# Optimization experiments

Hardware: AMD Instinct MI355X
Metric: run time of the kernel (lower is better)

## Reference

```python
import jax, jax.numpy as jnp
import numpy as np

I = 2048  # input_size
O = 2048  # output_size
K = 16    # number of parallel linears

def setup_inputs() -> dict:
    key = jax.random.key(0)
    ks = jax.random.split(key, 8)
    s_in = 1.0 / np.sqrt(I)
    s_cat = 1.0 / np.sqrt(K * O)
    x = jax.random.normal(ks[0], (4, 2048, I), dtype=jnp.float32)
    W16 = jax.random.uniform(ks[1], (K, O, I), jnp.float32, -s_in, s_in)   # stacked weights of 16 Linears
    b16 = jax.random.uniform(ks[2], (K, O), jnp.float32, -s_in, s_in)
    Wf = jax.random.uniform(ks[3], (O, K * O), jnp.float32, -s_cat, s_cat)  # fusion Linear weight
    bf = jax.random.uniform(ks[4], (O,), jnp.float32, -s_cat, s_cat)
    gamma = jnp.ones((O,), jnp.float32)  # LayerNorm weight
    beta = jnp.zeros((O,), jnp.float32)  # LayerNorm bias
    return {"x": x, "W16": W16, "b16": b16, "Wf": Wf, "bf": bf, "gamma": gamma, "beta": beta}

def reference(x, W16, b16, Wf, bf, gamma, beta):
    B, S, _ = x.shape
    # 16 parallel Linears as one batched GEMM; k index order == torch.cat order
    y = jnp.einsum('bsi,koi->bsko', x, W16) + b16          # [B,S,16,O]
    combined = y.reshape(B, S, K * O)                       # concat along last dim
    fused = jnp.einsum('bsc,oc->bso', combined, Wf) + bf    # fusion linear [B,S,O]
    # LayerNorm (eps=1e-5, torch default)
    mu = jnp.mean(fused, axis=-1, keepdims=True)
    var = jnp.mean(jnp.square(fused - mu), axis=-1, keepdims=True)
    normed = (fused - mu) * jax.lax.rsqrt(var + 1e-5) * gamma + beta
    # exact (erf) GELU matching torch nn.GELU default; dropout(p=0.005) is identity at eval
    return jax.nn.gelu(normed, approximate=False)
```

## Files before the change

kernel.cpp:

```cpp
#include <hip/hip_runtime.h>
#include <hip/hip_bf16.h>
#include <math.h>


typedef __bf16 bf16_t;
typedef __bf16 bf16x8 __attribute__((ext_vector_type(8)));
typedef __bf16 bf16x4 __attribute__((ext_vector_type(4)));
typedef float  f32x4  __attribute__((ext_vector_type(4)));

#define KC 32768
#define OD 2048
#define ID 2048
#define BSROWS 8192

#define GLL16(g, l) __builtin_amdgcn_global_load_lds( \
    (const __attribute__((address_space(1))) void*)(g), \
    (__attribute__((address_space(3))) void*)(l), 16, 0, 0)

__device__ __forceinline__ float wave_sum(float v) {
#pragma unroll
  for (int o = 32; o > 0; o >>= 1) v += __shfl_down(v, o, 64);
  return v;
}

__global__ __launch_bounds__(512, 1) void gemm256(
    const bf16_t* __restrict__ A, const bf16_t* __restrict__ B,
    float* __restrict__ C, int M, int N, int lda, int ldb,
    int Ks, int nbn, int mn)
{
  __shared__ char lds[131072];
  const int tid  = threadIdx.x;
  const int lane = tid & 63;
  const int wave = tid >> 6;

  const int nwg = gridDim.x;
  const int per = nwg >> 3;
  const int swz = (blockIdx.x & 7) * per + (blockIdx.x >> 3);
  const int z   = swz / mn;
  const int rem = swz - z * mn;
  const int bm  = (rem / nbn) * 256;
  const int bn  = (rem % nbn) * 256;
  const int k0  = z * Ks;
  float* Cz = C + (size_t)z * ((size_t)M * (size_t)N);

  const int wr = wave >> 2, wc = wave & 3;
  const int wrbase = wr * 128, wcbase = wc * 64;
  const int frow   = lane & 15;
  const int slot16 = (lane >> 4) * 16;

  const int srow = tid >> 2;
  const int scol = (tid & 3) * 8;
  const bf16_t* gA = A + (size_t)(bm + srow) * lda + k0 + scol;
  const bf16_t* gB = B + (size_t)(bn + srow) * ldb + k0 + scol;
  const int ldst = wave * 1024;

  f32x4 acc[8][4] = {};
  const int NC = Ks >> 5;

#define STAGE(c) do {                                             \
    char* Ab_ = lds + (((c) & 3) << 15);                          \
    char* Bb_ = Ab_ + 16384;                                      \
    const bf16_t* a_ = gA + (c) * 32;                             \
    const bf16_t* b_ = gB + (c) * 32;                             \
    GLL16(a_,                     Ab_ + ldst);                    \
    GLL16(a_ + (size_t)128 * lda, Ab_ + 8192 + ldst);             \
    GLL16(b_,                     Bb_ + ldst);                    \
    GLL16(b_ + (size_t)128 * ldb, Bb_ + 8192 + ldst);             \
  } while (0)

  STAGE(0); STAGE(1); STAGE(2);

  const int aoff = (wrbase + frow) * 64 + slot16;
  const int boff = (wcbase + frow) * 64 + slot16;

#pragma unroll 1
  for (int c = 0; c < NC; ++c) {
    if (c < NC - 2)       asm volatile("s_waitcnt vmcnt(8)" ::: "memory");
    else if (c == NC - 2) asm volatile("s_waitcnt vmcnt(4)" ::: "memory");
    else                  asm volatile("s_waitcnt vmcnt(0)" ::: "memory");
    __builtin_amdgcn_s_barrier();

    const char* ap = lds + ((c & 3) << 15) + aoff;
    const char* bp = lds + ((c & 3) << 15) + 16384 + boff;
    bf16x8 af[8], bg[4];
#pragma unroll
    for (int n = 0; n < 4; ++n)
      bg[n] = *reinterpret_cast<const bf16x8*>(bp + n * 1024);
#pragma unroll
    for (int m = 0; m < 8; ++m)
      af[m] = *reinterpret_cast<const bf16x8*>(ap + m * 1024);

    if (c + 3 < NC) STAGE(c + 3);

    __builtin_amdgcn_s_setprio(1);
#pragma unroll
    for (int m = 0; m < 8; ++m)
#pragma unroll
      for (int n = 0; n < 4; ++n)
        acc[m][n] = __builtin_amdgcn_mfma_f32_16x16x32_bf16(af[m], bg[n], acc[m][n], 0, 0, 0);
    __builtin_amdgcn_s_setprio(0);
  }
#undef STAGE

  const int cr = (lane >> 4) * 4, cc = lane & 15;
#pragma unroll
  for (int m = 0; m < 8; ++m)
#pragma unroll
    for (int n = 0; n < 4; ++n) {
      size_t base = (size_t)(bm + wrbase + m * 16 + cr) * N + (bn + wcbase + n * 16 + cc);
#pragma unroll
      for (int j = 0; j < 4; ++j)
        Cz[base + (size_t)j * N] = acc[m][n][j];
    }
}

__global__ void conv_wf_beq(const float* __restrict__ Wf, const float* __restrict__ b16,
                            bf16_t* __restrict__ Wf16, float* __restrict__ beq)
{
  const int o  = blockIdx.y;
  const int cb = blockIdx.x * 2048;
  const int t  = threadIdx.x;
  const size_t gbase = (size_t)o * KC + cb + t * 8;
  const float4 v0 = *(const float4*)(Wf + gbase);
  const float4 v1 = *(const float4*)(Wf + gbase + 4);
  const float4 b0 = *(const float4*)(b16 + cb + t * 8);
  const float4 b1 = *(const float4*)(b16 + cb + t * 8 + 4);
  bf16x8 r;
  r[0] = (bf16_t)v0.x; r[1] = (bf16_t)v0.y; r[2] = (bf16_t)v0.z; r[3] = (bf16_t)v0.w;
  r[4] = (bf16_t)v1.x; r[5] = (bf16_t)v1.y; r[6] = (bf16_t)v1.z; r[7] = (bf16_t)v1.w;
  *reinterpret_cast<bf16x8*>(Wf16 + gbase) = r;
  float s = v0.x * b0.x + v0.y * b0.y + v0.z * b0.z + v0.w * b0.w
          + v1.x * b1.x + v1.y * b1.y + v1.z * b1.z + v1.w * b1.w;
  s = wave_sum(s);
  __shared__ float red[4];
  if ((t & 63) == 0) red[t >> 6] = s;
  __syncthreads();
  if (t == 0) atomicAdd(beq + o, red[0] + red[1] + red[2] + red[3]);
}

__global__ void transpose_w16(const float* __restrict__ W, bf16_t* __restrict__ T)
{
  __shared__ bf16_t tile[64][65];
  const int cb = blockIdx.x * 64;
  const int ib = blockIdx.y * 64;
  const int tx = threadIdx.x & 63;
  const int ty = threadIdx.x >> 6;
#pragma unroll
  for (int r = ty; r < 64; r += 4)
    tile[r][tx] = (bf16_t)W[(size_t)(cb + r) * ID + ib + tx];
  __syncthreads();
#pragma unroll
  for (int r = ty; r < 64; r += 4)
    T[(size_t)(ib + r) * KC + cb + tx] = tile[tx][r];
}

__global__ void conv_x(const float* __restrict__ X, bf16_t* __restrict__ X16)
{
  const size_t i = ((size_t)blockIdx.x * 256 + threadIdx.x) * 8;
  const float4 v0 = *(const float4*)(X + i);
  const float4 v1 = *(const float4*)(X + i + 4);
  bf16x8 r;
  r[0] = (bf16_t)v0.x; r[1] = (bf16_t)v0.y; r[2] = (bf16_t)v0.z; r[3] = (bf16_t)v0.w;
  r[4] = (bf16_t)v1.x; r[5] = (bf16_t)v1.y; r[6] = (bf16_t)v1.z; r[7] = (bf16_t)v1.w;
  *reinterpret_cast<bf16x8*>(X16 + i) = r;
}

__global__ void reduce_weq(const float* __restrict__ slabs, bf16_t* __restrict__ Weq)
{
  const size_t MN = (size_t)OD * ID;
  const size_t i = ((size_t)blockIdx.x * 256 + threadIdx.x) * 4;
  float4 a = *(const float4*)(slabs + i);
  float4 b = *(const float4*)(slabs + MN + i);
  float4 c = *(const float4*)(slabs + 2 * MN + i);
  float4 d = *(const float4*)(slabs + 3 * MN + i);
  bf16x4 r;
  r[0] = (bf16_t)(a.x + b.x + c.x + d.x);
  r[1] = (bf16_t)(a.y + b.y + c.y + d.y);
  r[2] = (bf16_t)(a.z + b.z + c.z + d.z);
  r[3] = (bf16_t)(a.w + b.w + c.w + d.w);
  *reinterpret_cast<bf16x4*>(Weq + i) = r;
}

__global__ __launch_bounds__(256) void ln_gelu(
    const float* __restrict__ fused, const float* __restrict__ beq,
    const float* __restrict__ bfv, const float* __restrict__ gamma,
    const float* __restrict__ beta, float* __restrict__ out)
{
  const int row = blockIdx.x;
  const int t = threadIdx.x;
  const float* fr = fused + (size_t)row * OD;
  const int c0 = t * 8;
  float v[8];
  float s = 0.f, ss = 0.f;
#pragma unroll
  for (int j = 0; j < 2; ++j) {
    float4 x  = *(const float4*)(fr  + c0 + j * 4);
    float4 bq = *(const float4*)(beq + c0 + j * 4);
    float4 bb = *(const float4*)(bfv + c0 + j * 4);
    v[j * 4 + 0] = x.x + bq.x + bb.x;
    v[j * 4 + 1] = x.y + bq.y + bb.y;
    v[j * 4 + 2] = x.z + bq.z + bb.z;
    v[j * 4 + 3] = x.w + bq.w + bb.w;
#pragma unroll
    for (int e = 0; e < 4; ++e) { float w = v[j * 4 + e]; s += w; ss += w * w; }
  }
  s = wave_sum(s); ss = wave_sum(ss);
  __shared__ float rs[4], rss[4];
  if ((t & 63) == 0) { rs[t >> 6] = s; rss[t >> 6] = ss; }
  __syncthreads();
  const float S  = rs[0] + rs[1] + rs[2] + rs[3];
  const float SS = rss[0] + rss[1] + rss[2] + rss[3];
  const float mu   = S * (1.f / OD);
  const float var  = SS * (1.f / OD) - mu * mu;
  const float rstd = rsqrtf(var + 1e-5f);
#pragma unroll
  for (int j = 0; j < 2; ++j) {
    float4 g  = *(const float4*)(gamma + c0 + j * 4);
    float4 be = *(const float4*)(beta  + c0 + j * 4);
    float4 o;
    float xn;
    xn  = (v[j * 4 + 0] - mu) * rstd * g.x + be.x; o.x = 0.5f * xn * (1.f + erff(xn * 0.70710678118f));
    xn  = (v[j * 4 + 1] - mu) * rstd * g.y + be.y; o.y = 0.5f * xn * (1.f + erff(xn * 0.70710678118f));
    xn  = (v[j * 4 + 2] - mu) * rstd * g.z + be.z; o.z = 0.5f * xn * (1.f + erff(xn * 0.70710678118f));
    xn  = (v[j * 4 + 3] - mu) * rstd * g.w + be.w; o.w = 0.5f * xn * (1.f + erff(xn * 0.70710678118f));
    *(float4*)(out + (size_t)row * OD + c0 + j * 4) = o;
  }
}

extern "C" void kernel_launch(void* const* d_in, const int* in_sizes, int n_in,
                              void* d_out, int out_size, void* d_ws, size_t ws_size,
                              hipStream_t stream) {
  const float* x     = (const float*)d_in[0];
  const float* W16   = (const float*)d_in[1];
  const float* b16   = (const float*)d_in[2];
  const float* Wf    = (const float*)d_in[3];
  const float* bfv   = (const float*)d_in[4];
  const float* gamma = (const float*)d_in[5];
  const float* beta  = (const float*)d_in[6];
  float* out = (float*)d_out;

  char* ws = (char*)d_ws;
  bf16_t* W16T  = (bf16_t*)(ws);
  bf16_t* Wf16  = (bf16_t*)(ws + 134217728);
  bf16_t* X16   = (bf16_t*)(ws + 268435456);
  bf16_t* Weq   = (bf16_t*)(ws + 301989888);
  float*  beq   = (float*)(ws + 310378496);
  float*  slabs = (float*)(ws + 310386688);
  float*  fused = slabs;

  hipMemsetAsync(beq, 0, OD * sizeof(float), stream);

  conv_wf_beq<<<dim3(16, 2048), 256, 0, stream>>>(Wf, b16, Wf16, beq);
  transpose_w16<<<dim3(KC / 64, ID / 64), 256, 0, stream>>>(W16, W16T);
  conv_x<<<(BSROWS * ID) / (256 * 8), 256, 0, stream>>>(x, X16);

  gemm256<<<256, 512, 0, stream>>>(Wf16, W16T, slabs, OD, ID, KC, KC, KC / 4, 8, 64);
  reduce_weq<<<(OD * ID) / (256 * 4), 256, 0, stream>>>(slabs, Weq);

  gemm256<<<256, 512, 0, stream>>>(X16, Weq, fused, BSROWS, OD, ID, ID, ID, 8, 256);

  ln_gelu<<<BSROWS, 256, 0, stream>>>(fused, beq, bfv, gamma, beta, out);
}
```

Baseline: 623.7 us.

## Double-buffer LDS fragment reads in registers and deepen the global prefetch to four stages

The GEMM main loop now reads the next k-chunk's A/B fragments from LDS into a second register set while the MFMAs run on the current set. The global-to-LDS prefetch distance grows from three to four chunks, using all four LDS buffers, and the wait counts are adjusted to match. The aim is to hide LDS read latency behind MFMA work and keep more global loads in flight. In exchange it uses more VGPRs for the extra fragment set, and the loop assumes an even chunk count.

```diff
diff --git a/kernel.cpp b/kernel.cpp
--- a/kernel.cpp
+++ b/kernel.cpp
@@ -55,51 +55,68 @@
   const int ldst = wave * 1024;
 
   f32x4 acc[8][4] = {};
+  bf16x8 afA[8], bgA[4], afB[8], bgB[4];
   const int NC = Ks >> 5;
+
+  const int aoff = (wrbase + frow) * 64 + slot16;
+  const int boff = (wcbase + frow) * 64 + slot16;
 
 #define STAGE(c) do {                                             \
     char* Ab_ = lds + (((c) & 3) << 15);                          \
     char* Bb_ = Ab_ + 16384;                                      \
-    const bf16_t* a_ = gA + (c) * 32;                             \
-    const bf16_t* b_ = gB + (c) * 32;                             \
+    const bf16_t* a_ = gA + (size_t)(c) * 32;                     \
+    const bf16_t* b_ = gB + (size_t)(c) * 32;                     \
     GLL16(a_,                     Ab_ + ldst);                    \
     GLL16(a_ + (size_t)128 * lda, Ab_ + 8192 + ldst);             \
     GLL16(b_,                     Bb_ + ldst);                    \
     GLL16(b_ + (size_t)128 * ldb, Bb_ + 8192 + ldst);             \
   } while (0)
 
-  STAGE(0); STAGE(1); STAGE(2);
-
-  const int aoff = (wrbase + frow) * 64 + slot16;
-  const int boff = (wcbase + frow) * 64 + slot16;
+#define READ(c, af, bg) do {                                      \
+    const char* ap_ = lds + (((c) & 3) << 15) + aoff;             \
+    const char* bp_ = lds + (((c) & 3) << 15) + 16384 + boff;     \
+    _Pragma("unroll")                                             \
+    for (int n = 0; n < 4; ++n)                                   \
+      bg[n] = *reinterpret_cast<const bf16x8*>(bp_ + n * 1024);   \
+    _Pragma("unroll")                                             \
+    for (int m = 0; m < 8; ++m)                                   \
+      af[m] = *reinterpret_cast<const bf16x8*>(ap_ + m * 1024);   \
+  } while (0)
+
+#define MFMA32(af, bg) do {                                       \
+    __builtin_amdgcn_s_setprio(1);                                \
+    _Pragma("unroll")                                             \
+    for (int m = 0; m < 8; ++m)                                   \
+      _Pragma("unroll")                                           \
+      for (int n = 0; n < 4; ++n)                                 \
+        acc[m][n] = __builtin_amdgcn_mfma_f32_16x16x32_bf16(      \
+            af[m], bg[n], acc[m][n], 0, 0, 0);                    \
+    __builtin_amdgcn_s_setprio(0);                                \
+  } while (0)
+
+#define PHASE(c, afC, bgC, afN, bgN) do {                         \
+    if ((c) < NC - 3)       asm volatile("s_waitcnt vmcnt(8)" ::: "memory"); \
+    else if ((c) == NC - 3) asm volatile("s_waitcnt vmcnt(4)" ::: "memory"); \
+    else if ((c) == NC - 2) asm volatile("s_waitcnt vmcnt(0)" ::: "memory"); \
+    __builtin_amdgcn_s_barrier();                                 \
+    if ((c) + 4 < NC) STAGE((c) + 4);                             \
+    if ((c) + 1 < NC) READ((c) + 1, afN, bgN);                    \
+    MFMA32(afC, bgC);                                             \
+  } while (0)
+
+  STAGE(0); STAGE(1); STAGE(2); STAGE(3);
+  asm volatile("s_waitcnt vmcnt(12)" ::: "memory");
+  __builtin_amdgcn_s_barrier();
+  READ(0, afA, bgA);
 
 #pragma unroll 1
-  for (int c = 0; c < NC; ++c) {
-    if (c < NC - 2)       asm volatile("s_waitcnt vmcnt(8)" ::: "memory");
-    else if (c == NC - 2) asm volatile("s_waitcnt vmcnt(4)" ::: "memory");
-    else                  asm volatile("s_waitcnt vmcnt(0)" ::: "memory");
-    __builtin_amdgcn_s_barrier();
-
-    const char* ap = lds + ((c & 3) << 15) + aoff;
-    const char* bp = lds + ((c & 3) << 15) + 16384 + boff;
-    bf16x8 af[8], bg[4];
-#pragma unroll
-    for (int n = 0; n < 4; ++n)
-      bg[n] = *reinterpret_cast<const bf16x8*>(bp + n * 1024);
-#pragma unroll
-    for (int m = 0; m < 8; ++m)
-      af[m] = *reinterpret_cast<const bf16x8*>(ap + m * 1024);
-
-    if (c + 3 < NC) STAGE(c + 3);
-
-    __builtin_amdgcn_s_setprio(1);
-#pragma unroll
-    for (int m = 0; m < 8; ++m)
-#pragma unroll
-      for (int n = 0; n < 4; ++n)
-        acc[m][n] = __builtin_amdgcn_mfma_f32_16x16x32_bf16(af[m], bg[n], acc[m][n], 0, 0, 0);
-    __builtin_amdgcn_s_setprio(0);
+  for (int c = 0; c < NC; c += 2) {
+    PHASE(c,     afA, bgA, afB, bgB);
+    PHASE(c + 1, afB, bgB, afA, bgA);
   }
+#undef PHASE
+#undef MFMA32
+#undef READ
 #undef STAGE
 
   const int cr = (lane >> 4) * 4, cc = lane & 15;
```

New measurement: 600.3 us. 1.04x faster.

## Restructure GEMM main loop into 64-wide K tiles with phased LDS pipeline and swizzle

Applied to the files above, without the earlier changes.

The bf16 GEMM main loop moves from 32-wide K chunks with a 4-deep buffer to 64-wide K tiles, double-buffered in LDS. Each tile is processed in four phases that interleave global-to-LDS staging, register prefetch of the next A fragments and MFMAs, with an XOR-swizzled LDS layout meant to avoid bank conflicts. Separately, the weight transpose kernel now writes 16-byte vectorized rows instead of scalar bf16 stores. The aim is better overlap of memory and matrix work and fewer LDS conflicts, at the cost of more barriers per tile and more complex waitcnt logic that is easy to get wrong.

```diff
diff --git a/kernel.cpp b/kernel.cpp
--- a/kernel.cpp
+++ b/kernel.cpp
@@ -13,6 +13,11 @@
 #define ID 2048
 #define BSROWS 8192
 
+#define SEG_ALO 0
+#define SEG_AHI 16384
+#define SEG_BLO 32768
+#define SEG_BHI 49152
+
 #define GLL16(g, l) __builtin_amdgcn_global_load_lds( \
     (const __attribute__((address_space(1))) void*)(g), \
     (__attribute__((address_space(3))) void*)(l), 16, 0, 0)
@@ -35,73 +40,138 @@
 
   const int nwg = gridDim.x;
   const int per = nwg >> 3;
-  const int swz = (blockIdx.x & 7) * per + (blockIdx.x >> 3);
-  const int z   = swz / mn;
-  const int rem = swz - z * mn;
+  const int swzb = (blockIdx.x & 7) * per + (blockIdx.x >> 3);
+  const int z   = swzb / mn;
+  const int rem = swzb - z * mn;
   const int bm  = (rem / nbn) * 256;
   const int bn  = (rem % nbn) * 256;
   const int k0  = z * Ks;
   float* Cz = C + (size_t)z * ((size_t)M * (size_t)N);
 
   const int wr = wave >> 2, wc = wave & 3;
+  const int frow = lane & 15;
+
+  const int rdsl0 = ((((lane >> 4))    ^ (lane & 7)) * 16);
+  const int rdsl1 = ((((lane >> 4) + 4) ^ (lane & 7)) * 16);
+
+  const int srow8 = lane >> 3;
+  const int scole = ((lane & 7) ^ srow8) * 8;
+  const bf16_t* gAs = A + (size_t)(bm + srow8) * lda + k0 + scole;
+  const bf16_t* gBs = B + (size_t)(bn + srow8) * ldb + k0 + scole;
+
+  const int abase = wr * 16384 + frow * 128;
+  const int bbase = 32768 + (wc >> 1) * 16384 + ((wc & 1) * 64 + frow) * 128;
+
+  f32x4 acc[8][4] = {};
+  bf16x8 aA[2][2], aB[2][2], bA[4][2], bB[4][2];
+  const int NT = Ks >> 6;
+
+#define STAGEH(g, ld, segoff, tile, halfbase) do {                        \
+    const bf16_t* s_ = (g) + (size_t)((halfbase) + 16 * wave) * (ld)      \
+                           + (size_t)(tile) * 64;                         \
+    char* d_ = lds + (((tile) & 1) << 16) + (segoff) + wave * 2048;       \
+    GLL16(s_,                    d_);                                     \
+    GLL16(s_ + (size_t)8 * (ld), d_ + 1024);                              \
+  } while (0)
+
+#define READA(tile, q, ar) do {                                           \
+    const char* p_ = lds + (((tile) & 1) << 16) + abase + (q) * 4096;     \
+    _Pragma("unroll") for (int mh = 0; mh < 2; ++mh) {                    \
+      ar[mh][0] = *reinterpret_cast<const bf16x8*>(p_ + mh*2048 + rdsl0); \
+      ar[mh][1] = *reinterpret_cast<const bf16x8*>(p_ + mh*2048 + rdsl1); \
+    }                                                                     \
+  } while (0)
+
+#define READB(tile, bg) do {                                              \
+    const char* p_ = lds + (((tile) & 1) << 16) + bbase;                  \
+    _Pragma("unroll") for (int n = 0; n < 4; ++n) {                       \
+      bg[n][0] = *reinterpret_cast<const bf16x8*>(p_ + n*2048 + rdsl0);   \
+      bg[n][1] = *reinterpret_cast<const bf16x8*>(p_ + n*2048 + rdsl1);   \
+    }                                                                     \
+  } while (0)
+
+#define MFMAQ(p, ac, bc) do {                                             \
+    __builtin_amdgcn_s_setprio(1);                                        \
+    _Pragma("unroll") for (int mh = 0; mh < 2; ++mh)                      \
+      _Pragma("unroll") for (int n = 0; n < 4; ++n) {                     \
+        acc[2*(p)+mh][n] = __builtin_amdgcn_mfma_f32_16x16x32_bf16(       \
+            ac[mh][0], bc[n][0], acc[2*(p)+mh][n], 0, 0, 0);              \
+        acc[2*(p)+mh][n] = __builtin_amdgcn_mfma_f32_16x16x32_bf16(       \
+            ac[mh][1], bc[n][1], acc[2*(p)+mh][n], 0, 0, 0);              \
+      }                                                                   \
+    __builtin_amdgcn_s_setprio(0);                                        \
+  } while (0)
+
+#define ENDPH() do {                                                      \
+    asm volatile("s_waitcnt lgkmcnt(0)" ::: "memory");                    \
+    __builtin_amdgcn_sched_barrier(0);                                    \
+    __builtin_amdgcn_s_barrier();                                         \
+  } while (0)
+
+#define PH0(t, ac, an, bc) do {                                           \
+    if ((t) + 2 < NT) STAGEH(gBs, ldb, SEG_BLO, (t)+2, 0);                \
+    READA((t), 1, an);                                                    \
+    MFMAQ(0, ac, bc);                                                     \
+    ENDPH();                                                              \
+  } while (0)
+#define PH1(t, ac, an, bc) do {                                           \
+    if ((t) + 2 < NT) STAGEH(gBs, ldb, SEG_BHI, (t)+2, 128);              \
+    READA((t), 2, an);                                                    \
+    MFMAQ(1, ac, bc);                                                     \
+    ENDPH();                                                              \
+  } while (0)
+#define PH2(t, ac, an, bc) do {                                           \
+    READA((t), 3, an);                                                    \
+    MFMAQ(2, ac, bc);                                                     \
+    ENDPH();                                                              \
+  } while (0)
+#define PH3(t, ac, an, bc, bn) do {                                       \
+    if ((t) + 1 < NT) {                                                   \
+      if ((t) + 2 < NT) asm volatile("s_waitcnt vmcnt(4)" ::: "memory");  \
+      else              asm volatile("s_waitcnt vmcnt(0)" ::: "memory");  \
+      __builtin_amdgcn_s_barrier();   \
+    }                                                                     \
+    if ((t) + 2 < NT) { STAGEH(gAs, lda, SEG_ALO, (t)+2, 0);              \
+                        STAGEH(gAs, lda, SEG_AHI, (t)+2, 128); }          \
+    if ((t) + 1 < NT) { READA((t)+1, 0, an); READB((t)+1, bn); }          \
+    MFMAQ(3, ac, bc);                                                     \
+    ENDPH();                                                              \
+  } while (0)
+
+  STAGEH(gBs, ldb, SEG_BLO, 0, 0);   STAGEH(gBs, ldb, SEG_BHI, 0, 128);
+  STAGEH(gAs, lda, SEG_ALO, 0, 0);   STAGEH(gAs, lda, SEG_AHI, 0, 128);
+  STAGEH(gBs, ldb, SEG_BLO, 1, 0);   STAGEH(gBs, ldb, SEG_BHI, 1, 128);
+  STAGEH(gAs, lda, SEG_ALO, 1, 0);   STAGEH(gAs, lda, SEG_AHI, 1, 128);
+  asm volatile("s_waitcnt vmcnt(8)" ::: "memory");
+  __builtin_amdgcn_s_barrier();
+  READB(0, bA);
+  READA(0, 0, aA);
+  asm volatile("s_waitcnt lgkmcnt(0)" ::: "memory");
+  __builtin_amdgcn_sched_barrier(0);
+  __builtin_amdgcn_s_barrier();
+
+#pragma unroll 1
+  for (int t = 0; t < NT; t += 2) {
+    PH0(t,     aA, aB, bA);
+    PH1(t,     aB, aA, bA);
+    PH2(t,     aA, aB, bA);
+    PH3(t,     aB, aA, bA, bB);
+    PH0(t + 1, aA, aB, bB);
+    PH1(t + 1, aB, aA, bB);
+    PH2(t + 1, aA, aB, bB);
+    PH3(t + 1, aB, aA, bB, bA);
+  }
+#undef PH0
+#undef PH1
+#undef PH2
+#undef PH3
+#undef ENDPH
+#undef MFMAQ
+#undef READB
+#undef READA
+#undef STAGEH
+
   const int wrbase = wr * 128, wcbase = wc * 64;
-  const int frow   = lane & 15;
-  const int slot16 = (lane >> 4) * 16;
-
-  const int srow = tid >> 2;
-  const int scol = (tid & 3) * 8;
-  const bf16_t* gA = A + (size_t)(bm + srow) * lda + k0 + scol;
-  const bf16_t* gB = B + (size_t)(bn + srow) * ldb + k0 + scol;
-  const int ldst = wave * 1024;
-
-  f32x4 acc[8][4] = {};
-  const int NC = Ks >> 5;
-
-#define STAGE(c) do {                                             \
-    char* Ab_ = lds + (((c) & 3) << 15);                          \
-    char* Bb_ = Ab_ + 16384;                                      \
-    const bf16_t* a_ = gA + (c) * 32;                             \
-    const bf16_t* b_ = gB + (c) * 32;                             \
-    GLL16(a_,                     Ab_ + ldst);                    \
-    GLL16(a_ + (size_t)128 * lda, Ab_ + 8192 + ldst);             \
-    GLL16(b_,                     Bb_ + ldst);                    \
-    GLL16(b_ + (size_t)128 * ldb, Bb_ + 8192 + ldst);             \
-  } while (0)
-
-  STAGE(0); STAGE(1); STAGE(2);
-
-  const int aoff = (wrbase + frow) * 64 + slot16;
-  const int boff = (wcbase + frow) * 64 + slot16;
-
-#pragma unroll 1
-  for (int c = 0; c < NC; ++c) {
-    if (c < NC - 2)       asm volatile("s_waitcnt vmcnt(8)" ::: "memory");
-    else if (c == NC - 2) asm volatile("s_waitcnt vmcnt(4)" ::: "memory");
-    else                  asm volatile("s_waitcnt vmcnt(0)" ::: "memory");
-    __builtin_amdgcn_s_barrier();
-
-    const char* ap = lds + ((c & 3) << 15) + aoff;
-    const char* bp = lds + ((c & 3) << 15) + 16384 + boff;
-    bf16x8 af[8], bg[4];
-#pragma unroll
-    for (int n = 0; n < 4; ++n)
-      bg[n] = *reinterpret_cast<const bf16x8*>(bp + n * 1024);
-#pragma unroll
-    for (int m = 0; m < 8; ++m)
-      af[m] = *reinterpret_cast<const bf16x8*>(ap + m * 1024);
-
-    if (c + 3 < NC) STAGE(c + 3);
-
-    __builtin_amdgcn_s_setprio(1);
-#pragma unroll
-    for (int m = 0; m < 8; ++m)
-#pragma unroll
-      for (int n = 0; n < 4; ++n)
-        acc[m][n] = __builtin_amdgcn_mfma_f32_16x16x32_bf16(af[m], bg[n], acc[m][n], 0, 0, 0);
-    __builtin_amdgcn_s_setprio(0);
-  }
-#undef STAGE
-
   const int cr = (lane >> 4) * 4, cc = lane & 15;
 #pragma unroll
   for (int m = 0; m < 8; ++m)
@@ -149,9 +219,16 @@
   for (int r = ty; r < 64; r += 4)
     tile[r][tx] = (bf16_t)W[(size_t)(cb + r) * ID + ib + tx];
   __syncthreads();
-#pragma unroll
-  for (int r = ty; r < 64; r += 4)
-    T[(size_t)(ib + r) * KC + cb + tx] = tile[tx][r];
+  const int orow = threadIdx.x >> 3;
+  const int oc8  = (threadIdx.x & 7) * 8;
+#pragma unroll
+  for (int rr = 0; rr < 2; ++rr) {
+    const int r = orow + rr * 32;
+    bf16x8 v;
+#pragma unroll
+    for (int j = 0; j < 8; ++j) v[j] = tile[oc8 + j][r];
+    *reinterpret_cast<bf16x8*>(T + (size_t)(ib + r) * KC + cb + oc8) = v;
+  }
 }
 
 __global__ void conv_x(const float* __restrict__ X, bf16_t* __restrict__ X16)
```

New measurement: 676.9 us. 8.5% more time.

## Restructure GEMM mainloop with 64-wide K tiles, swizzled LDS, and phased prefetch

Applied to the files above, without the earlier changes.

Rewrites the bf16 MFMA GEMM mainloop to use 64-element K tiles with an XOR-swizzled LDS layout, so fragment reads avoid bank conflicts. A and B are staged in half-tile phases, and B fragments for the next tile are prefetched into double-buffered registers while the current tile's MFMAs run. The transpose_w16 kernel now writes 16-byte vectorized bf16 rows instead of scalar stores. The new schedule adds more barriers and hand-tuned waitcnt logic, which raises register pressure and the risk of synchronization mistakes.

```diff
diff --git a/kernel.cpp b/kernel.cpp
--- a/kernel.cpp
+++ b/kernel.cpp
@@ -44,64 +44,127 @@
   float* Cz = C + (size_t)z * ((size_t)M * (size_t)N);
 
   const int wr = wave >> 2, wc = wave & 3;
+  const int frow  = lane & 15;
+  const int bhalf = wc >> 1;
+
+  const int rdsl0 = (((lane >> 4))     ^ (lane & 7)) * 16;
+  const int rdsl1 = (((lane >> 4) + 4) ^ (lane & 7)) * 16;
+
+  const int abase = wr * 16384 + frow * 128;
+  const int bloc  = ((wc & 1) * 64 + frow) * 128;
+
+  const int srow8 = tid >> 3;
+  const int sw8   = (tid & 7) ^ (srow8 & 7);
+  const bf16_t* gA0 = A + (size_t)(bm + srow8) * lda + k0 + sw8 * 8;
+  const bf16_t* gB0 = B + (size_t)(bn + srow8) * ldb + k0 + sw8 * 8;
+  const int ldw = wave * 1024;
+
+  f32x4 acc[8][4] = {};
+  bf16x8 aqE[2][2], aqO[2][2], bA[4][2], bB[4][2];
+  const int NT = Ks >> 6;
+
+#define STAGE_A_HALF(t, hf) do {                                          \
+    _Pragma("unroll") for (int s_ = 0; s_ < 2; ++s_)                      \
+      GLL16(gA0 + (size_t)((hf) * 128 + s_ * 64) * lda + (size_t)(t) * 64,\
+            lds + (((t) & 1) << 15) + (hf) * 16384 + s_ * 8192 + ldw);    \
+  } while (0)
+
+#define STAGE_B_HALF(t, hh) do {                                          \
+    _Pragma("unroll") for (int s_ = 0; s_ < 2; ++s_)                      \
+      GLL16(gB0 + (size_t)((hh) * 128 + s_ * 64) * ldb + (size_t)(t) * 64,\
+            lds + 65536 + ((((t) * 2 + (hh)) & 3) << 14) + s_ * 8192 + ldw); \
+  } while (0)
+
+#define READ_AQ(t, q, aq) do {                                            \
+    const char* p_ = lds + (((t) & 1) << 15) + abase + (q) * 4096;        \
+    aq[0][0] = *reinterpret_cast<const bf16x8*>(p_ + rdsl0);              \
+    aq[0][1] = *reinterpret_cast<const bf16x8*>(p_ + rdsl1);              \
+    aq[1][0] = *reinterpret_cast<const bf16x8*>(p_ + 2048 + rdsl0);       \
+    aq[1][1] = *reinterpret_cast<const bf16x8*>(p_ + 2048 + rdsl1);       \
+  } while (0)
+
+#define READ_BH(t, kh, bg) do {                                           \
+    const char* p_ = lds + 65536 + ((((t) * 2 + bhalf) & 3) << 14) + bloc;\
+    _Pragma("unroll") for (int n_ = 0; n_ < 4; ++n_)                      \
+      bg[n_][kh] = *reinterpret_cast<const bf16x8*>(                      \
+          p_ + n_ * 2048 + ((kh) ? rdsl1 : rdsl0));                       \
+  } while (0)
+
+#define SYNCPH() do {                                                     \
+    __builtin_amdgcn_s_barrier();                                         \
+    asm volatile("s_waitcnt lgkmcnt(0)" ::: "memory");                    \
+    __builtin_amdgcn_sched_barrier(0);                                    \
+  } while (0)
+
+#define MFMA_Q(q, aq, bg) do {                                            \
+    __builtin_amdgcn_s_setprio(1);                                        \
+    _Pragma("unroll") for (int mh_ = 0; mh_ < 2; ++mh_)                   \
+      _Pragma("unroll") for (int n_ = 0; n_ < 4; ++n_) {                  \
+        acc[2*(q)+mh_][n_] = __builtin_amdgcn_mfma_f32_16x16x32_bf16(     \
+            aq[mh_][0], bg[n_][0], acc[2*(q)+mh_][n_], 0, 0, 0);          \
+        acc[2*(q)+mh_][n_] = __builtin_amdgcn_mfma_f32_16x16x32_bf16(     \
+            aq[mh_][1], bg[n_][1], acc[2*(q)+mh_][n_], 0, 0, 0);          \
+      }                                                                   \
+    __builtin_amdgcn_s_setprio(0);                                        \
+  } while (0)
+
+#define TILE(t, BC, BN) do {                                              \
+                                                                  \
+    if ((t) + 1 < NT) STAGE_A_HALF((t) + 1, 0);                           \
+    READ_AQ((t), 0, aqE);                                                 \
+    SYNCPH(); MFMA_Q(0, aqE, BC);                                         \
+                                                                  \
+    if ((t) + 1 < NT) STAGE_A_HALF((t) + 1, 1);                           \
+    READ_AQ((t), 1, aqO);                                                 \
+    SYNCPH(); MFMA_Q(1, aqO, BC);                                         \
+    if ((t) + 1 < NT) {                \
+      asm volatile("s_waitcnt vmcnt(4)" ::: "memory");                    \
+      __builtin_amdgcn_s_barrier();                                       \
+    }                                                                     \
+                                                                  \
+    if ((t) + 2 < NT) STAGE_B_HALF((t) + 2, 0);                           \
+    READ_AQ((t), 2, aqE);                                                 \
+    if ((t) + 1 < NT) READ_BH((t) + 1, 0, BN);                            \
+    SYNCPH(); MFMA_Q(2, aqE, BC);                                         \
+                                                                  \
+    if ((t) + 2 < NT) STAGE_B_HALF((t) + 2, 1);                           \
+    READ_AQ((t), 3, aqO);                                                 \
+    if ((t) + 1 < NT) READ_BH((t) + 1, 1, BN);                            \
+    SYNCPH(); MFMA_Q(3, aqO, BC);                                         \
+    if ((t) + 2 < NT) {                \
+      asm volatile("s_waitcnt vmcnt(4)" ::: "memory");                    \
+      __builtin_amdgcn_s_barrier();                                       \
+    } else if ((t) + 1 < NT) {                                            \
+      asm volatile("s_waitcnt vmcnt(0)" ::: "memory");    \
+      __builtin_amdgcn_s_barrier();                                       \
+    }                                                                     \
+  } while (0)
+
+  STAGE_A_HALF(0, 0); STAGE_A_HALF(0, 1);
+  STAGE_B_HALF(0, 0); STAGE_B_HALF(0, 1);
+  STAGE_B_HALF(1, 0); STAGE_B_HALF(1, 1);
+  asm volatile("s_waitcnt vmcnt(4)" ::: "memory");
+  __builtin_amdgcn_s_barrier();
+  READ_BH(0, 0, bA);
+  READ_BH(0, 1, bA);
+  asm volatile("s_waitcnt lgkmcnt(0)" ::: "memory");
+  __builtin_amdgcn_sched_barrier(0);
+  __builtin_amdgcn_s_barrier();
+
+#pragma unroll 1
+  for (int t = 0; t < NT; t += 2) {
+    TILE(t,     bA, bB);
+    TILE(t + 1, bB, bA);
+  }
+#undef TILE
+#undef MFMA_Q
+#undef SYNCPH
+#undef READ_BH
+#undef READ_AQ
+#undef STAGE_B_HALF
+#undef STAGE_A_HALF
+
   const int wrbase = wr * 128, wcbase = wc * 64;
-  const int frow   = lane & 15;
-  const int slot16 = (lane >> 4) * 16;
-
-  const int srow = tid >> 2;
-  const int scol = (tid & 3) * 8;
-  const bf16_t* gA = A + (size_t)(bm + srow) * lda + k0 + scol;
-  const bf16_t* gB = B + (size_t)(bn + srow) * ldb + k0 + scol;
-  const int ldst = wave * 1024;
-
-  f32x4 acc[8][4] = {};
-  const int NC = Ks >> 5;
-
-#define STAGE(c) do {                                             \
-    char* Ab_ = lds + (((c) & 3) << 15);                          \
-    char* Bb_ = Ab_ + 16384;                                      \
-    const bf16_t* a_ = gA + (c) * 32;                             \
-    const bf16_t* b_ = gB + (c) * 32;                             \
-    GLL16(a_,                     Ab_ + ldst);                    \
-    GLL16(a_ + (size_t)128 * lda, Ab_ + 8192 + ldst);             \
-    GLL16(b_,                     Bb_ + ldst);                    \
-    GLL16(b_ + (size_t)128 * ldb, Bb_ + 8192 + ldst);             \
-  } while (0)
-
-  STAGE(0); STAGE(1); STAGE(2);
-
-  const int aoff = (wrbase + frow) * 64 + slot16;
-  const int boff = (wcbase + frow) * 64 + slot16;
-
-#pragma unroll 1
-  for (int c = 0; c < NC; ++c) {
-    if (c < NC - 2)       asm volatile("s_waitcnt vmcnt(8)" ::: "memory");
-    else if (c == NC - 2) asm volatile("s_waitcnt vmcnt(4)" ::: "memory");
-    else                  asm volatile("s_waitcnt vmcnt(0)" ::: "memory");
-    __builtin_amdgcn_s_barrier();
-
-    const char* ap = lds + ((c & 3) << 15) + aoff;
-    const char* bp = lds + ((c & 3) << 15) + 16384 + boff;
-    bf16x8 af[8], bg[4];
-#pragma unroll
-    for (int n = 0; n < 4; ++n)
-      bg[n] = *reinterpret_cast<const bf16x8*>(bp + n * 1024);
-#pragma unroll
-    for (int m = 0; m < 8; ++m)
-      af[m] = *reinterpret_cast<const bf16x8*>(ap + m * 1024);
-
-    if (c + 3 < NC) STAGE(c + 3);
-
-    __builtin_amdgcn_s_setprio(1);
-#pragma unroll
-    for (int m = 0; m < 8; ++m)
-#pragma unroll
-      for (int n = 0; n < 4; ++n)
-        acc[m][n] = __builtin_amdgcn_mfma_f32_16x16x32_bf16(af[m], bg[n], acc[m][n], 0, 0, 0);
-    __builtin_amdgcn_s_setprio(0);
-  }
-#undef STAGE
-
   const int cr = (lane >> 4) * 4, cc = lane & 15;
 #pragma unroll
   for (int m = 0; m < 8; ++m)
@@ -149,9 +212,16 @@
   for (int r = ty; r < 64; r += 4)
     tile[r][tx] = (bf16_t)W[(size_t)(cb + r) * ID + ib + tx];
   __syncthreads();
-#pragma unroll
-  for (int r = ty; r < 64; r += 4)
-    T[(size_t)(ib + r) * KC + cb + tx] = tile[tx][r];
+  const int orow = threadIdx.x >> 3;
+  const int oc8  = (threadIdx.x & 7) * 8;
+#pragma unroll
+  for (int rr = 0; rr < 2; ++rr) {
+    const int r = orow + rr * 32;
+    bf16x8 v;
+#pragma unroll
+    for (int j = 0; j < 8; ++j) v[j] = tile[oc8 + j][r];
+    *reinterpret_cast<bf16x8*>(T + (size_t)(ib + r) * KC + cb + oc8) = v;
+  }
 }
 
 __global__ void conv_x(const float* __restrict__ X, bf16_t* __restrict__ X16)
```

New measurement: 537.0 us. 1.16x faster.
